# Performance work log

Hardware: AMD Instinct MI355X
Metric: run time of the kernel (lower is better)

Reference implementation:

```python
import jax, jax.numpy as jnp
import numpy as np
import math

B, N, CS, CZ, H, C, P, PV, NB = 1, 512, 384, 128, 12, 16, 4, 8, 64


def quat_to_rot(q):
    q = q / jnp.clip(jnp.linalg.norm(q, axis=-1, keepdims=True), 1e-8)
    w, x, y, z = q[..., 0], q[..., 1], q[..., 2], q[..., 3]
    return jnp.stack([
        w*w + x*x - y*y - z*z, 2*(x*y - w*z), 2*(x*z + w*y),
        2*(x*y + w*z), w*w - x*x + y*y - z*z, 2*(y*z - w*x),
        2*(x*z - w*y), 2*(y*z + w*x), w*w - x*x - y*y + z*z,
    ], axis=-1).reshape(q.shape[:-1] + (3, 3))


def setup_inputs() -> dict:
    key = jax.random.key(0)
    ks = jax.random.split(key, 28)
    def n(k, shape, sc=1.0):
        return jax.random.normal(k, shape, jnp.float32) * sc
    s = n(ks[0], (B, N, CS))
    z = n(ks[1], (B, N, N, CZ))
    translations = n(ks[2], (B, N, 3)) * 4.0  # spread distances over 0-32A bins
    rotations = quat_to_rot(n(ks[3], (B, N, 4)))  # valid SO(3) frames
    mask = jnp.ones((B, N), dtype=bool)
    inv = lambda fan: 1.0 / math.sqrt(fan)
    return {
        's': s, 'z': z, 'translations': translations, 'rotations': rotations, 'mask': mask,
        'Wq': n(ks[4], (CS, H*C), inv(CS)), 'bq': n(ks[5], (H*C,), 0.01),
        'Wk': n(ks[6], (CS, H*C), inv(CS)), 'bk': n(ks[7], (H*C,), 0.01),
        'Wv': n(ks[8], (CS, H*C), inv(CS)), 'bv': n(ks[9], (H*C,), 0.01),
        'Wqp': n(ks[10], (CS, H*P*3), inv(CS)), 'bqp': n(ks[11], (H*P*3,), 0.01),
        'Wkp': n(ks[12], (CS, H*P*3), inv(CS)), 'bkp': n(ks[13], (H*P*3,), 0.01),
        'Wvp': n(ks[14], (CS, H*PV*3), inv(CS)), 'bvp': n(ks[15], (H*PV*3,), 0.01),
        'Wb': n(ks[16], (CZ, H), inv(CZ)), 'bb': n(ks[17], (H,), 0.01),
        'dist_emb': n(ks[18], (NB, H), 0.02),
        'scale_logits': n(ks[19], (3, H), 0.1),
        'head_weights': jnp.abs(n(ks[20], (H,))) * 0.2 + 0.8,
        'Wout': n(ks[21], (H*(C + PV*4 + CZ), CS), inv(H*(C + PV*4 + CZ))),
        'bout': n(ks[22], (CS,), 0.01),
    }


def reference(s, z, translations, rotations, mask, Wq, bq, Wk, bk, Wv, bv,
              Wqp, bqp, Wkp, bkp, Wvp, bvp, Wb, bb, dist_emb, scale_logits,
              head_weights, Wout, bout):
    b, n, _ = s.shape
    q = (s @ Wq + bq).reshape(b, n, H, C)
    k = (s @ Wk + bk).reshape(b, n, H, C)
    v = (s @ Wv + bv).reshape(b, n, H, C)
    q_pts = (s @ Wqp + bqp).reshape(b, n, H, P, 3)
    k_pts = (s @ Wkp + bkp).reshape(b, n, H, P, 3)
    v_pts = (s @ Wvp + bvp).reshape(b, n, H, PV, 3)
    t = translations[:, :, None, None, :]
    q_g = jnp.einsum('bnij,bnhpj->bnhpi', rotations, q_pts) + t
    k_g = jnp.einsum('bnij,bnhpj->bnhpi', rotations, k_pts) + t
    v_g = jnp.einsum('bnij,bnhpj->bnhpi', rotations, v_pts) + t
    scalar_logits = jnp.einsum('bnhc,bmhc->bnmh', q, k) / math.sqrt(C)
    # squared point distances, summed over points p and coords i, via expansion
    q_sq = (q_g**2).sum((-1, -2))  # (b, n, h)
    k_sq = (k_g**2).sum((-1, -2))
    cross = jnp.einsum('bnhpi,bmhpi->bnmh', q_g, k_g)
    point_dist = q_sq[:, :, None, :] + k_sq[:, None, :, :] - 2.0 * cross
    point_logits = -0.5 * point_dist * head_weights
    pair_bias = z @ Wb + bb  # (b, n, m, h)
    pair_dist = jnp.linalg.norm(
        translations[:, :, None, :] - translations[:, None, :, :], axis=-1)
    edges = jnp.linspace(0.0, 32.0, NB + 1)
    bins = jnp.clip(jnp.searchsorted(edges, pair_dist, side='left') - 1, 0, NB - 1)
    dist_bias = dist_emb[bins]
    local = (pair_dist <= 5.0).astype(s.dtype)
    medium = ((pair_dist > 5.0) & (pair_dist <= 15.0)).astype(s.dtype)
    scales = jnp.stack([local, medium, jnp.ones_like(pair_dist)], axis=-1)
    per_head = jax.nn.softmax(scale_logits, axis=0)  # (3, h)
    multiscale = jnp.einsum('bnms,sh->bnmh', scales, per_head)
    logits = scalar_logits + point_logits + pair_bias + dist_bias + multiscale
    m2d = mask[:, :, None] & mask[:, None, :]
    logits = jnp.where(m2d[..., None], logits, -10000.0)
    attn = jax.nn.softmax(logits.astype(jnp.float32), axis=2).astype(s.dtype)
    out_scalar = jnp.einsum('bnmh,bmhc->bnhc', attn, v)
    out_pts_g = jnp.einsum('bnmh,bmhpi->bnhpi', attn, v_g)
    out_pts_l = jnp.einsum('bnji,bnhpj->bnhpi', rotations, out_pts_g - t)  # R^T x
    out_norms = jnp.linalg.norm(out_pts_l, axis=-1)  # (b, n, h, pv)
    pair_feat = jnp.einsum('bnmh,bnmc->bnhc', attn, z)
    feats = jnp.concatenate(
        [out_scalar, out_pts_l.reshape(b, n, H, PV * 3), out_norms, pair_feat],
        axis=-1).reshape(b, n, -1)
    return feats @ Wout + bout
```

## Files before the change

kernel.cpp:

```cpp
#include <hip/hip_runtime.h>
#include <math.h>

#define N   512
#define CS  384
#define CZ  128
#define H   12
#define C   16
#define P   4
#define PV  8
#define NB  64
#define KSP 528
#define QKD 28
#define QPAD 68
#define APAD 516

#define OFF_Q    0
#define OFF_K    98304
#define OFF_V    196608
#define OFF_QP   294912
#define OFF_KP   368640
#define OFF_VP   442368
#define OFF_QG   589824
#define OFF_KG   663552
#define OFF_VG   737280
#define OFF_QSQ  884736
#define OFF_KSQ  890880
#define OFF_LOG  897024
#define OFF_FEAT 4042752

__global__ __launch_bounds__(256) void k_proj(
    const float* __restrict__ s,
    const float* __restrict__ Wq,  const float* __restrict__ bq,
    const float* __restrict__ Wk,  const float* __restrict__ bk,
    const float* __restrict__ Wv,  const float* __restrict__ bv,
    const float* __restrict__ Wqp, const float* __restrict__ bqp,
    const float* __restrict__ Wkp, const float* __restrict__ bkp,
    const float* __restrict__ Wvp, const float* __restrict__ bvp,
    float* __restrict__ ws)
{
    __shared__ float s_s[16*388];
    const int tid = threadIdx.x;
    const int n0  = blockIdx.y * 16;
    const int gc  = blockIdx.x * 64 + (tid & 15) * 4;
    const int nl  = tid >> 4;
    for (int i = tid; i < 16*384; i += 256) {
        int r = i / 384, c = i - r*384;
        s_s[r*388 + c] = s[(n0 + r)*384 + c];
    }
    __syncthreads();
    const float* W; const float* b; float* dst; int width; int lc;
    if      (gc < 192) { W=Wq;  b=bq;  width=192; lc=gc;     dst=ws+OFF_Q;  }
    else if (gc < 384) { W=Wk;  b=bk;  width=192; lc=gc-192; dst=ws+OFF_K;  }
    else if (gc < 576) { W=Wv;  b=bv;  width=192; lc=gc-384; dst=ws+OFF_V;  }
    else if (gc < 720) { W=Wqp; b=bqp; width=144; lc=gc-576; dst=ws+OFF_QP; }
    else if (gc < 864) { W=Wkp; b=bkp; width=144; lc=gc-720; dst=ws+OFF_KP; }
    else               { W=Wvp; b=bvp; width=288; lc=gc-864; dst=ws+OFF_VP; }
    float4 acc = {0.f,0.f,0.f,0.f};
    const float* wp   = W + lc;
    const float* srow = s_s + nl*388;
    #pragma unroll 8
    for (int kk = 0; kk < 384; kk++) {
        float4 w4 = *(const float4*)(wp + (size_t)kk*width);
        float  sv = srow[kk];
        acc.x += sv*w4.x; acc.y += sv*w4.y; acc.z += sv*w4.z; acc.w += sv*w4.w;
    }
    float4 b4 = *(const float4*)(b + lc);
    acc.x += b4.x; acc.y += b4.y; acc.z += b4.z; acc.w += b4.w;
    *(float4*)(dst + (size_t)(n0+nl)*width + lc) = acc;
}

__global__ __launch_bounds__(192) void k_frames(
    const float* __restrict__ rot, const float* __restrict__ trans,
    float* __restrict__ ws)
{
    int n = blockIdx.x, tid = threadIdx.x;
    __shared__ float R[9], T[3], qg_s[144], kg_s[144];
    if (tid < 9) R[tid] = rot[n*9 + tid];
    if (tid < 3) T[tid] = trans[n*3 + tid];
    __syncthreads();
    if (tid < 48) {
        const float* lp = ws + OFF_QP + n*144 + tid*3;
        float l0=lp[0], l1=lp[1], l2=lp[2];
        float* gp = ws + OFF_QG + n*144 + tid*3;
        for (int i=0;i<3;i++){ float g = R[i*3+0]*l0 + R[i*3+1]*l1 + R[i*3+2]*l2 + T[i]; gp[i]=g; qg_s[tid*3+i]=g; }
    } else if (tid < 96) {
        int u = tid-48;
        const float* lp = ws + OFF_KP + n*144 + u*3;
        float l0=lp[0], l1=lp[1], l2=lp[2];
        float* gp = ws + OFF_KG + n*144 + u*3;
        for (int i=0;i<3;i++){ float g = R[i*3+0]*l0 + R[i*3+1]*l1 + R[i*3+2]*l2 + T[i]; gp[i]=g; kg_s[u*3+i]=g; }
    } else {
        int u = tid-96;
        const float* lp = ws + OFF_VP + n*288 + u*3;
        float l0=lp[0], l1=lp[1], l2=lp[2];
        float* gp = ws + OFF_VG + n*288 + u*3;
        for (int i=0;i<3;i++){ float g = R[i*3+0]*l0 + R[i*3+1]*l1 + R[i*3+2]*l2 + T[i]; gp[i]=g; }
    }
    __syncthreads();
    if (tid < 12) {
        float a=0;
        for (int d=0; d<12; d++){ float x=qg_s[tid*12+d]; a+=x*x; }
        ws[OFF_QSQ + n*12 + tid]=a;
    } else if (tid < 24) {
        int h = tid-12; float a=0;
        for (int d=0; d<12; d++){ float x=kg_s[h*12+d]; a+=x*x; }
        ws[OFF_KSQ + n*12 + h]=a;
    }
}

__global__ __launch_bounds__(256) void k_qkpt(
    const float* __restrict__ head_weights, float* __restrict__ ws)
{
    __shared__ float qs[QKD*QPAD], ks[QKD*QPAD], qa[64], kb[64];
    const int tid = threadIdx.x;
    const int m0 = blockIdx.x * 64, n0 = blockIdx.y * 64, h = blockIdx.z;
    const float hw = head_weights[h];
    for (int idx = tid; idx < 64*16; idx += 256) {
        int r = idx >> 4, c = idx & 15;
        qs[c*QPAD + r] = ws[OFF_Q + (n0+r)*192 + h*16 + c] * 0.25f;
        ks[c*QPAD + r] = ws[OFF_K + (m0+r)*192 + h*16 + c];
    }
    for (int idx = tid; idx < 64*12; idx += 256) {
        int r = idx / 12, c = idx % 12;
        qs[(16+c)*QPAD + r] = ws[OFF_QG + (n0+r)*144 + h*12 + c] * hw;
        ks[(16+c)*QPAD + r] = ws[OFF_KG + (m0+r)*144 + h*12 + c];
    }
    for (int idx = tid; idx < 64; idx += 256) {
        qa[idx] = -0.5f * hw * ws[OFF_QSQ + (n0+idx)*12 + h];
        kb[idx] = -0.5f * hw * ws[OFF_KSQ + (m0+idx)*12 + h];
    }
    __syncthreads();
    const int tx = tid & 15, ty = tid >> 4;
    float acc[4][4] = {{0.f}};
    #pragma unroll 4
    for (int d = 0; d < QKD; d++) {
        float4 a = *(const float4*)(qs + d*QPAD + ty*4);
        float4 b = *(const float4*)(ks + d*QPAD + tx*4);
        const float* ap = &a.x; const float* bp = &b.x;
        #pragma unroll
        for (int i=0;i<4;i++)
            #pragma unroll
            for (int j=0;j<4;j++) acc[i][j] += ap[i]*bp[j];
    }
    #pragma unroll
    for (int i=0;i<4;i++) {
        float ai = qa[ty*4+i];
        float4 r;
        r.x = acc[i][0] + ai + kb[tx*4+0];
        r.y = acc[i][1] + ai + kb[tx*4+1];
        r.z = acc[i][2] + ai + kb[tx*4+2];
        r.w = acc[i][3] + ai + kb[tx*4+3];
        *(float4*)(ws + OFF_LOG + ((size_t)(n0+ty*4+i)*H + h)*N + m0 + tx*4) = r;
    }
}

__global__ __launch_bounds__(256) void k_zbias(
    const float* __restrict__ z, const float* __restrict__ trans,
    const float* __restrict__ Wb, const float* __restrict__ bb,
    const float* __restrict__ dist_emb, const float* __restrict__ scale_logits,
    float* __restrict__ ws)
{
    const int n = blockIdx.y;
    const int m = blockIdx.x * 256 + threadIdx.x;
    float dx = trans[n*3+0]-trans[m*3+0];
    float dy = trans[n*3+1]-trans[m*3+1];
    float dz = trans[n*3+2]-trans[m*3+2];
    float pd = sqrtf(dx*dx+dy*dy+dz*dz);
    int bin = (int)ceilf(2.f*pd) - 1;
    bin = bin < 0 ? 0 : (bin > NB-1 ? NB-1 : bin);
    const float4 de0 = *(const float4*)(dist_emb + bin*12);
    const float4 de1 = *(const float4*)(dist_emb + bin*12 + 4);
    const float4 de2 = *(const float4*)(dist_emb + bin*12 + 8);
    float de[12] = {de0.x,de0.y,de0.z,de0.w, de1.x,de1.y,de1.z,de1.w, de2.x,de2.y,de2.z,de2.w};
    float acc[12];
    #pragma unroll
    for (int h=0; h<12; h++) {
        float a = scale_logits[0*H+h], b = scale_logits[1*H+h], c = scale_logits[2*H+h];
        float mx = fmaxf(a, fmaxf(b,c));
        float ea=__expf(a-mx), eb=__expf(b-mx), ec=__expf(c-mx);
        float inv = 1.f/(ea+eb+ec);
        float msc = ec*inv;
        if (pd <= 5.f)       msc += ea*inv;
        else if (pd <= 15.f) msc += eb*inv;
        acc[h] = bb[h] + de[h] + msc;
    }
    const float* zp = z + ((size_t)n*N + m)*CZ;
    #pragma unroll 2
    for (int c4 = 0; c4 < CZ/4; c4++) {
        float4 z4 = *(const float4*)(zp + c4*4);
        const float* zv = &z4.x;
        #pragma unroll
        for (int j=0; j<4; j++)
            #pragma unroll
            for (int h=0; h<12; h++)
                acc[h] += zv[j] * Wb[(c4*4+j)*H + h];
    }
    float* lp = ws + OFF_LOG + (size_t)n*H*N + m;
    #pragma unroll
    for (int h=0; h<12; h++)
        lp[(size_t)h*N] += acc[h];
}

__global__ __launch_bounds__(256) void k_pairz(
    const float* __restrict__ z, float* __restrict__ ws)
{
    __shared__ float attn_s[H*APAD];
    __shared__ float part[4*12*64];
    const int ch = blockIdx.x, n = blockIdx.y;
    const int tid = threadIdx.x;
    const int lane = tid & 63, wave = tid >> 6;

    const float4* asrc = (const float4*)(ws + OFF_LOG + (size_t)n*H*N);
    for (int i = tid; i < H*(N/4); i += 256) {
        int h = i >> 7, q = i & 127;
        *(float4*)(attn_s + h*APAD + q*4) = asrc[h*128 + q];
    }
    __syncthreads();
    for (int h = wave; h < H; h += 4) {
        float* row = attn_s + h*APAD;
        float v[8]; float mx = -1e30f;
        #pragma unroll
        for (int j=0;j<8;j++){ v[j]=row[lane + j*64]; mx = fmaxf(mx, v[j]); }
        #pragma unroll
        for (int off=32; off>0; off>>=1) mx = fmaxf(mx, __shfl_xor(mx, off, 64));
        float sum = 0.f;
        #pragma unroll
        for (int j=0;j<8;j++){ v[j]=__expf(v[j]-mx); sum += v[j]; }
        #pragma unroll
        for (int off=32; off>0; off>>=1) sum += __shfl_xor(sum, off, 64);
        float inv = 1.f/sum;
        #pragma unroll
        for (int j=0;j<8;j++) row[lane + j*64] = v[j]*inv;
    }
    __syncthreads();

    const int cq = tid & 15;
    const int ms = tid >> 4;
    const float* zb = z + (size_t)n*N*CZ + ch*64 + cq*4;
    float4 acc[12];
    #pragma unroll
    for (int h=0; h<12; h++) acc[h] = make_float4(0.f,0.f,0.f,0.f);
    const int r0 = ms*32;
    #pragma unroll 2
    for (int rq = 0; rq < 8; rq++) {
        const int r = r0 + rq*4;
        float4 z0 = *(const float4*)(zb + (size_t)(r+0)*CZ);
        float4 z1 = *(const float4*)(zb + (size_t)(r+1)*CZ);
        float4 z2 = *(const float4*)(zb + (size_t)(r+2)*CZ);
        float4 z3 = *(const float4*)(zb + (size_t)(r+3)*CZ);
        #pragma unroll
        for (int h=0; h<12; h++) {
            float4 a4 = *(const float4*)(attn_s + h*APAD + r);
            acc[h].x += a4.x*z0.x + a4.y*z1.x + a4.z*z2.x + a4.w*z3.x;
            acc[h].y += a4.x*z0.y + a4.y*z1.y + a4.z*z2.y + a4.w*z3.y;
            acc[h].z += a4.x*z0.z + a4.y*z1.z + a4.z*z2.z + a4.w*z3.z;
            acc[h].w += a4.x*z0.w + a4.y*z1.w + a4.z*z2.w + a4.w*z3.w;
        }
    }
    #pragma unroll
    for (int h=0; h<12; h++) {
        acc[h].x += __shfl_xor(acc[h].x, 16, 64); acc[h].y += __shfl_xor(acc[h].y, 16, 64);
        acc[h].z += __shfl_xor(acc[h].z, 16, 64); acc[h].w += __shfl_xor(acc[h].w, 16, 64);
        acc[h].x += __shfl_xor(acc[h].x, 32, 64); acc[h].y += __shfl_xor(acc[h].y, 32, 64);
        acc[h].z += __shfl_xor(acc[h].z, 32, 64); acc[h].w += __shfl_xor(acc[h].w, 32, 64);
    }
    if (lane < 16) {
        #pragma unroll
        for (int h=0; h<12; h++)
            *(float4*)(part + (wave*12 + h)*64 + lane*4) = acc[h];
    }
    __syncthreads();
    if (tid < 192) {
        const int h = tid >> 4, c4 = tid & 15;
        float4 s = *(const float4*)(part + (0*12 + h)*64 + c4*4);
        #pragma unroll
        for (int w=1; w<4; w++) {
            float4 p = *(const float4*)(part + (w*12 + h)*64 + c4*4);
            s.x += p.x; s.y += p.y; s.z += p.z; s.w += p.w;
        }
        *(float4*)(ws + OFF_FEAT + (size_t)n*2112 + h*176 + 48 + ch*64 + c4*4) = s;
    }
}

__global__ __launch_bounds__(256) void k_attnA(
    const float* __restrict__ rot, const float* __restrict__ trans,
    float* __restrict__ ws)
{
    __shared__ float attn_s[H*APAD];
    __shared__ float part[240*4];
    __shared__ float og_s[288];
    const int n = blockIdx.x, tid = threadIdx.x;
    const int lane = tid & 63, wave = tid >> 6;

    const float4* asrc = (const float4*)(ws + OFF_LOG + (size_t)n*H*N);
    for (int i = tid; i < H*(N/4); i += 256) {
        int h = i >> 7, q = i & 127;
        *(float4*)(attn_s + h*APAD + q*4) = asrc[h*128 + q];
    }
    __syncthreads();
    for (int h = wave; h < H; h += 4) {
        float* row = attn_s + h*APAD;
        float v[8]; float mx = -1e30f;
        #pragma unroll
        for (int j=0;j<8;j++){ v[j]=row[lane + j*64]; mx = fmaxf(mx, v[j]); }
        #pragma unroll
        for (int off=32; off>0; off>>=1) mx = fmaxf(mx, __shfl_xor(mx, off, 64));
        float sum = 0.f;
        #pragma unroll
        for (int j=0;j<8;j++){ v[j]=__expf(v[j]-mx); sum += v[j]; }
        #pragma unroll
        for (int off=32; off>0; off>>=1) sum += __shfl_xor(sum, off, 64);
        float inv = 1.f/sum;
        #pragma unroll
        for (int j=0;j<8;j++) row[lane + j*64] = v[j]*inv;
    }
    __syncthreads();

    if (tid < 240) {
        const int col4 = (tid % 120) * 4;
        const int msA  = tid / 120;
        const float* aptr; int astride, ah;
        if (col4 < 192) { ah = col4 >> 4;        aptr = ws + OFF_V  + col4;       astride = 192; }
        else            { ah = (col4-192) / 24;  aptr = ws + OFF_VG + (col4-192); astride = 288; }
        const float4* arow = (const float4*)(attn_s + ah*APAD);
        float4 acc = {0.f,0.f,0.f,0.f};
        #pragma unroll 2
        for (int mq = msA*64; mq < msA*64 + 64; mq++) {
            float4 a4 = arow[mq];
            const float* vp = aptr + (size_t)mq*4*astride;
            float4 v0 = *(const float4*)(vp);
            float4 v1 = *(const float4*)(vp + astride);
            float4 v2 = *(const float4*)(vp + 2*astride);
            float4 v3 = *(const float4*)(vp + 3*astride);
            acc.x += a4.x*v0.x + a4.y*v1.x + a4.z*v2.x + a4.w*v3.x;
            acc.y += a4.x*v0.y + a4.y*v1.y + a4.z*v2.y + a4.w*v3.y;
            acc.z += a4.x*v0.z + a4.y*v1.z + a4.z*v2.z + a4.w*v3.z;
            acc.w += a4.x*v0.w + a4.y*v1.w + a4.z*v2.w + a4.w*v3.w;
        }
        *(float4*)(part + tid*4) = acc;
    }
    __syncthreads();
    if (tid < 120) {
        const int col4 = tid * 4;
        float4 a = *(const float4*)(part + tid*4);
        float4 b = *(const float4*)(part + (tid+120)*4);
        a.x += b.x; a.y += b.y; a.z += b.z; a.w += b.w;
        if (col4 < 192) {
            const int ah = col4 >> 4;
            *(float4*)(ws + OFF_FEAT + (size_t)n*2112 + ah*176 + (col4 & 15)) = a;
        } else {
            *(float4*)(og_s + (col4 - 192)) = a;
        }
    }
    __syncthreads();
    if (tid < 96) {
        const int h = tid >> 3, p = tid & 7;
        float g0 = og_s[h*24 + p*3 + 0] - trans[n*3+0];
        float g1 = og_s[h*24 + p*3 + 1] - trans[n*3+1];
        float g2 = og_s[h*24 + p*3 + 2] - trans[n*3+2];
        const float* R = rot + n*9;
        float* fdst = ws + OFF_FEAT + (size_t)n*2112 + h*176;
        float nsq = 0.f;
        #pragma unroll
        for (int i=0;i<3;i++){
            float l = R[0*3+i]*g0 + R[1*3+i]*g1 + R[2*3+i]*g2;
            fdst[16 + p*3 + i] = l;
            nsq += l*l;
        }
        fdst[40 + p] = sqrtf(nsq);
    }
}

__global__ __launch_bounds__(384) void k_bias(
    const float* __restrict__ bout, float* __restrict__ out)
{
    out[(size_t)blockIdx.x*CS + threadIdx.x] = bout[threadIdx.x];
}

__global__ __launch_bounds__(256) void k_out(
    const float* __restrict__ Wout, const float* __restrict__ ws,
    float* __restrict__ out)
{
    __shared__ float f_s[16*KSP];
    const int tid = threadIdx.x;
    const int n0  = blockIdx.y * 16;
    const int k0  = blockIdx.z * KSP;
    const int col = blockIdx.x * 64 + (tid & 15) * 4;
    const int nl  = tid >> 4;
    for (int i = tid; i < 16*KSP; i += 256) {
        int r = i / KSP, c = i - r*KSP;
        f_s[i] = ws[OFF_FEAT + (size_t)(n0 + r)*2112 + k0 + c];
    }
    __syncthreads();
    float4 acc = {0.f,0.f,0.f,0.f};
    const float* wp   = Wout + (size_t)k0*CS + col;
    const float* frow = f_s + nl*KSP;
    #pragma unroll 8
    for (int kk = 0; kk < KSP; kk++) {
        float4 w4 = *(const float4*)(wp + (size_t)kk*CS);
        float  fv = frow[kk];
        acc.x += fv*w4.x; acc.y += fv*w4.y; acc.z += fv*w4.z; acc.w += fv*w4.w;
    }
    float* o = out + (size_t)(n0+nl)*CS + col;
    atomicAdd(o+0, acc.x); atomicAdd(o+1, acc.y);
    atomicAdd(o+2, acc.z); atomicAdd(o+3, acc.w);
}

extern "C" void kernel_launch(void* const* d_in, const int* in_sizes, int n_in,
                              void* d_out, int out_size, void* d_ws, size_t ws_size,
                              hipStream_t stream) {
    const float* s     = (const float*)d_in[0];
    const float* z     = (const float*)d_in[1];
    const float* trans = (const float*)d_in[2];
    const float* rot   = (const float*)d_in[3];
    const float* Wq  = (const float*)d_in[5];  const float* bq  = (const float*)d_in[6];
    const float* Wk  = (const float*)d_in[7];  const float* bk  = (const float*)d_in[8];
    const float* Wv  = (const float*)d_in[9];  const float* bv  = (const float*)d_in[10];
    const float* Wqp = (const float*)d_in[11]; const float* bqp = (const float*)d_in[12];
    const float* Wkp = (const float*)d_in[13]; const float* bkp = (const float*)d_in[14];
    const float* Wvp = (const float*)d_in[15]; const float* bvp = (const float*)d_in[16];
    const float* Wb  = (const float*)d_in[17]; const float* bb  = (const float*)d_in[18];
    const float* dist_emb     = (const float*)d_in[19];
    const float* scale_logits = (const float*)d_in[20];
    const float* head_weights = (const float*)d_in[21];
    const float* Wout = (const float*)d_in[22]; const float* bout = (const float*)d_in[23];
    float* out = (float*)d_out;
    float* ws  = (float*)d_ws;

    k_proj<<<dim3(18, 32), 256, 0, stream>>>(s, Wq,bq, Wk,bk, Wv,bv, Wqp,bqp, Wkp,bkp, Wvp,bvp, ws);
    k_frames<<<N, 192, 0, stream>>>(rot, trans, ws);
    k_qkpt<<<dim3(8, 8, 12), 256, 0, stream>>>(head_weights, ws);
    k_zbias<<<dim3(2, 512), 256, 0, stream>>>(z, trans, Wb, bb, dist_emb, scale_logits, ws);
    k_pairz<<<dim3(2, 512), 256, 0, stream>>>(z, ws);
    k_attnA<<<N, 256, 0, stream>>>(rot, trans, ws);
    k_bias<<<N, CS, 0, stream>>>(bout, out);
    k_out<<<dim3(6, 32, 4), 256, 0, stream>>>(Wout, ws, out);
}
```

Measured before the change: 414.7 us.

## Register-block 4 rows per thread with split-K reduction in projection and output GEMMs

```diff
diff --git a/kernel.cpp b/kernel.cpp
--- a/kernel.cpp
+++ b/kernel.cpp
@@ -39,34 +39,62 @@
     float* __restrict__ ws)
 {
     __shared__ float s_s[16*388];
+    __shared__ float part[4*16*68];
     const int tid = threadIdx.x;
     const int n0  = blockIdx.y * 16;
-    const int gc  = blockIdx.x * 64 + (tid & 15) * 4;
-    const int nl  = tid >> 4;
+    const int cq  = tid & 15;
+    const int rg  = (tid >> 4) & 3;
+    const int ks  = tid >> 6;
+    const int gc  = blockIdx.x * 64 + cq * 4;
     for (int i = tid; i < 16*384; i += 256) {
         int r = i / 384, c = i - r*384;
         s_s[r*388 + c] = s[(n0 + r)*384 + c];
     }
     __syncthreads();
-    const float* W; const float* b; float* dst; int width; int lc;
-    if      (gc < 192) { W=Wq;  b=bq;  width=192; lc=gc;     dst=ws+OFF_Q;  }
-    else if (gc < 384) { W=Wk;  b=bk;  width=192; lc=gc-192; dst=ws+OFF_K;  }
-    else if (gc < 576) { W=Wv;  b=bv;  width=192; lc=gc-384; dst=ws+OFF_V;  }
-    else if (gc < 720) { W=Wqp; b=bqp; width=144; lc=gc-576; dst=ws+OFF_QP; }
-    else if (gc < 864) { W=Wkp; b=bkp; width=144; lc=gc-720; dst=ws+OFF_KP; }
-    else               { W=Wvp; b=bvp; width=288; lc=gc-864; dst=ws+OFF_VP; }
-    float4 acc = {0.f,0.f,0.f,0.f};
-    const float* wp   = W + lc;
-    const float* srow = s_s + nl*388;
-    #pragma unroll 8
-    for (int kk = 0; kk < 384; kk++) {
+    const float* W; int width; int lc;
+    if      (gc < 192) { W=Wq;  width=192; lc=gc;     }
+    else if (gc < 384) { W=Wk;  width=192; lc=gc-192; }
+    else if (gc < 576) { W=Wv;  width=192; lc=gc-384; }
+    else if (gc < 720) { W=Wqp; width=144; lc=gc-576; }
+    else if (gc < 864) { W=Wkp; width=144; lc=gc-720; }
+    else               { W=Wvp; width=288; lc=gc-864; }
+    float acc[4][4] = {{0.f}};
+    const float* wp   = W + lc + (size_t)(ks*96)*width;
+    const float* srow = s_s + (rg*4)*388 + ks*96;
+    #pragma unroll 4
+    for (int kk = 0; kk < 96; kk++) {
         float4 w4 = *(const float4*)(wp + (size_t)kk*width);
-        float  sv = srow[kk];
-        acc.x += sv*w4.x; acc.y += sv*w4.y; acc.z += sv*w4.z; acc.w += sv*w4.w;
-    }
-    float4 b4 = *(const float4*)(b + lc);
-    acc.x += b4.x; acc.y += b4.y; acc.z += b4.z; acc.w += b4.w;
-    *(float4*)(dst + (size_t)(n0+nl)*width + lc) = acc;
+        #pragma unroll
+        for (int r = 0; r < 4; r++) {
+            float sv = srow[r*388 + kk];
+            acc[r][0] += sv*w4.x; acc[r][1] += sv*w4.y;
+            acc[r][2] += sv*w4.z; acc[r][3] += sv*w4.w;
+        }
+    }
+    #pragma unroll
+    for (int r = 0; r < 4; r++)
+        *(float4*)(part + (ks*16 + rg*4 + r)*68 + cq*4) =
+            make_float4(acc[r][0], acc[r][1], acc[r][2], acc[r][3]);
+    __syncthreads();
+    {
+        const int row = tid >> 4;
+        float4 sum = *(const float4*)(part + (0*16 + row)*68 + cq*4);
+        #pragma unroll
+        for (int k2 = 1; k2 < 4; k2++) {
+            float4 p = *(const float4*)(part + (k2*16 + row)*68 + cq*4);
+            sum.x += p.x; sum.y += p.y; sum.z += p.z; sum.w += p.w;
+        }
+        const float* b; float* dst; int w2, lc2;
+        if      (gc < 192) { b=bq;  w2=192; lc2=gc;     dst=ws+OFF_Q;  }
+        else if (gc < 384) { b=bk;  w2=192; lc2=gc-192; dst=ws+OFF_K;  }
+        else if (gc < 576) { b=bv;  w2=192; lc2=gc-384; dst=ws+OFF_V;  }
+        else if (gc < 720) { b=bqp; w2=144; lc2=gc-576; dst=ws+OFF_QP; }
+        else if (gc < 864) { b=bkp; w2=144; lc2=gc-720; dst=ws+OFF_KP; }
+        else               { b=bvp; w2=288; lc2=gc-864; dst=ws+OFF_VP; }
+        float4 b4 = *(const float4*)(b + lc2);
+        sum.x += b4.x; sum.y += b4.y; sum.z += b4.z; sum.w += b4.w;
+        *(float4*)(dst + (size_t)(n0+row)*w2 + lc2) = sum;
+    }
 }
 
 __global__ __launch_bounds__(192) void k_frames(
@@ -382,28 +410,49 @@
     float* __restrict__ out)
 {
     __shared__ float f_s[16*KSP];
+    __shared__ float part[4*16*68];
     const int tid = threadIdx.x;
     const int n0  = blockIdx.y * 16;
     const int k0  = blockIdx.z * KSP;
-    const int col = blockIdx.x * 64 + (tid & 15) * 4;
-    const int nl  = tid >> 4;
+    const int cq  = tid & 15;
+    const int rg  = (tid >> 4) & 3;
+    const int ks  = tid >> 6;
+    const int col = blockIdx.x * 64 + cq * 4;
     for (int i = tid; i < 16*KSP; i += 256) {
         int r = i / KSP, c = i - r*KSP;
         f_s[i] = ws[OFF_FEAT + (size_t)(n0 + r)*2112 + k0 + c];
     }
     __syncthreads();
-    float4 acc = {0.f,0.f,0.f,0.f};
-    const float* wp   = Wout + (size_t)k0*CS + col;
-    const float* frow = f_s + nl*KSP;
-    #pragma unroll 8
-    for (int kk = 0; kk < KSP; kk++) {
+    float acc[4][4] = {{0.f}};
+    const float* wp = Wout + (size_t)(k0 + ks*132)*CS + col;
+    const float* f0 = f_s + (rg*4)*KSP + ks*132;
+    #pragma unroll 4
+    for (int kk = 0; kk < 132; kk++) {
         float4 w4 = *(const float4*)(wp + (size_t)kk*CS);
-        float  fv = frow[kk];
-        acc.x += fv*w4.x; acc.y += fv*w4.y; acc.z += fv*w4.z; acc.w += fv*w4.w;
-    }
-    float* o = out + (size_t)(n0+nl)*CS + col;
-    atomicAdd(o+0, acc.x); atomicAdd(o+1, acc.y);
-    atomicAdd(o+2, acc.z); atomicAdd(o+3, acc.w);
+        #pragma unroll
+        for (int r = 0; r < 4; r++) {
+            float fv = f0[r*KSP + kk];
+            acc[r][0] += fv*w4.x; acc[r][1] += fv*w4.y;
+            acc[r][2] += fv*w4.z; acc[r][3] += fv*w4.w;
+        }
+    }
+    #pragma unroll
+    for (int r = 0; r < 4; r++)
+        *(float4*)(part + (ks*16 + rg*4 + r)*68 + cq*4) =
+            make_float4(acc[r][0], acc[r][1], acc[r][2], acc[r][3]);
+    __syncthreads();
+    {
+        const int row = tid >> 4;
+        float4 s = *(const float4*)(part + (0*16 + row)*68 + cq*4);
+        #pragma unroll
+        for (int k2 = 1; k2 < 4; k2++) {
+            float4 p = *(const float4*)(part + (k2*16 + row)*68 + cq*4);
+            s.x += p.x; s.y += p.y; s.z += p.z; s.w += p.w;
+        }
+        float* o = out + (size_t)(n0+row)*CS + col;
+        atomicAdd(o+0, s.x); atomicAdd(o+1, s.y);
+        atomicAdd(o+2, s.z); atomicAdd(o+3, s.w);
+    }
 }
 
 extern "C" void kernel_launch(void* const* d_in, const int* in_sizes, int n_in,
```

New measurement: 368.8 us. 1.12x faster.
